# Optimization experiments

Measured on AMD Instinct MI355X. Metric: run time of the kernel, lower is better.

## Reference

```python
import jax, jax.numpy as jnp
import numpy as np

EMBED_DIM = 1024


def setup_inputs() -> dict:
    key = jax.random.key(0)
    ks = jax.random.split(key, 8)
    B, S, D = 4, 2048, EMBED_DIM
    scale = 1.0 / np.sqrt(D)
    x = jax.random.normal(ks[0], (B, S, D), dtype=jnp.float32)
    mask = jnp.zeros((S, S), dtype=jnp.float32)
    # nn.Linear default init ~ U(-1/sqrt(fan_in), 1/sqrt(fan_in)); exact dist irrelevant for correctness
    w_q = jax.random.uniform(ks[1], (D, D), jnp.float32, -scale, scale)
    b_q = jax.random.uniform(ks[2], (D,), jnp.float32, -scale, scale)
    w_k = jax.random.uniform(ks[3], (D, D), jnp.float32, -scale, scale)
    b_k = jax.random.uniform(ks[4], (D,), jnp.float32, -scale, scale)
    w_v = jax.random.uniform(ks[5], (D, D), jnp.float32, -scale, scale)
    b_v = jax.random.uniform(ks[6], (D,), jnp.float32, -scale, scale)
    return {"x": x, "mask": mask, "w_q": w_q, "b_q": b_q,
            "w_k": w_k, "b_k": b_k, "w_v": w_v, "b_v": b_v}


def reference(x, mask, w_q, b_q, w_k, b_k, w_v, b_v):
    D = x.shape[-1]
    # nn.Linear computes x @ W^T + b
    Q = jnp.einsum('bsd,ed->bse', x, w_q) + b_q
    K = jnp.einsum('bsd,ed->bse', x, w_k) + b_k
    V = jnp.einsum('bsd,ed->bse', x, w_v) + b_v
    scores = jnp.einsum('bqd,bkd->bqk', Q, K) / jnp.sqrt(jnp.asarray(D, x.dtype))
    scores = scores + mask  # additive mask, broadcast over batch
    attn = jax.nn.softmax(scores, axis=-1)
    return jnp.einsum('bqk,bkd->bqd', attn, V)
```

## Files before the change

kernel.cpp:

```cpp
#include <hip/hip_runtime.h>


typedef __attribute__((ext_vector_type(8))) short short8;
typedef __attribute__((ext_vector_type(4))) short short4v;
typedef __attribute__((ext_vector_type(4))) float float4v;

__device__ __forceinline__ short f2bf(float f) {
  unsigned u = __builtin_bit_cast(unsigned, f);
  u += 0x7fffu + ((u >> 16) & 1u);
  return (short)(u >> 16);
}

__device__ __forceinline__ void gl2lds16(const void* g, void* l) {
  __builtin_amdgcn_global_load_lds((const __attribute__((address_space(1))) void*)g,
                                   (__attribute__((address_space(3))) void*)l, 16, 0, 0);
}

__global__ __launch_bounds__(256) void cvt_kernel(const float* __restrict__ in,
                                                  short* __restrict__ out, int n4) {
  int i = blockIdx.x * 256 + threadIdx.x;
  if (i < n4) {
    float4v v = ((const float4v*)in)[i];
    short4v o;
    o.x = f2bf(v.x); o.y = f2bf(v.y); o.z = f2bf(v.z); o.w = f2bf(v.w);
    ((short4v*)out)[i] = o;
  }
}

__global__ __launch_bounds__(256) void prep_kernel(const float* __restrict__ wq,
                                                   const float* __restrict__ wk,
                                                   const float* __restrict__ wv,
                                                   const float* __restrict__ bq,
                                                   const float* __restrict__ bk,
                                                   const float* __restrict__ bv,
                                                   short* __restrict__ w_bf,
                                                   float* __restrict__ bcat) {
  int b = blockIdx.x;
  if (b < 3072) {
    int seg = b >> 10;
    const float* w = seg == 0 ? wq : (seg == 1 ? wk : wv);
    int i = (b - (seg << 10)) * 256 + threadIdx.x;
    float4v v = ((const float4v*)w)[i];
    short4v o;
    o.x = f2bf(v.x); o.y = f2bf(v.y); o.z = f2bf(v.z); o.w = f2bf(v.w);
    ((short4v*)(w_bf + (long)seg * 1048576))[i] = o;
  } else {
    int i = (b - 3072) * 256 + threadIdx.x;
    if (i < 3072) bcat[i] = i < 1024 ? bq[i] : (i < 2048 ? bk[i - 1024] : bv[i - 2048]);
  }
}

template <int EPI>
__global__ __launch_bounds__(256) void gemm_bt(const short* __restrict__ Aall,
                                               const short* __restrict__ Ball,
                                               void* __restrict__ Call,
                                               const float* __restrict__ aux, float scale,
                                               int M, int N, int Kd,
                                               long ab, long bb, long cb, long auxb) {
  const int bz = blockIdx.z;
  const short* A = Aall + (long)bz * ab;
  const short* Bm = Ball + (long)bz * bb;
  const float* auxp = aux + (long)bz * auxb;

  const int m0 = blockIdx.x * 128;
  const int n0 = blockIdx.y * 128;

  __shared__ alignas(16) short As[128][64];
  __shared__ alignas(16) short Bs[128][64];

  const int t = threadIdx.x;
  const int lane = t & 63, wave = t >> 6;
  const int wm = (wave & 1) * 64, wn = (wave >> 1) * 64;
  const int col = lane & 15, quad = lane >> 4;

  const int r_loc = lane >> 3;
  const int slot = lane & 7;
  const int cch = slot ^ r_loc;
  const int sw = col & 7;

  float4v acc[4][4] = {};
  float4v lacc[4] = {};
  short8 ones;
  if (EPI == 2) {
#pragma unroll
    for (int e = 0; e < 8; ++e) ones[e] = (short)0x3F80;
  }

  for (int kt = 0; kt < Kd; kt += 64) {
#pragma unroll
    for (int u = 0; u < 4; ++u) {
      const int rowbase = wave * 32 + u * 8;
      const int r = rowbase + r_loc;
      const long goff = (long)r * Kd + kt + cch * 8;
      short* lA = &As[rowbase][0] + lane * 8;
      short* lB = &Bs[rowbase][0] + lane * 8;
      gl2lds16(&A[(long)m0 * Kd + goff], lA);
      gl2lds16(&Bm[(long)n0 * Kd + goff], lB);
    }
    __syncthreads();

#pragma unroll
    for (int s = 0; s < 2; ++s) {
      short8 af[4], bfr[4];
#pragma unroll
      for (int i = 0; i < 4; ++i)
        af[i] = *(const short8*)&As[wm + i * 16 + col][((s * 4 + quad) ^ sw) * 8];
#pragma unroll
      for (int j = 0; j < 4; ++j)
        bfr[j] = *(const short8*)&Bs[wn + j * 16 + col][((s * 4 + quad) ^ sw) * 8];
#pragma unroll
      for (int i = 0; i < 4; ++i) {
#pragma unroll
        for (int j = 0; j < 4; ++j)
          acc[i][j] = __builtin_amdgcn_mfma_f32_16x16x32_bf16(af[i], bfr[j], acc[i][j], 0, 0, 0);
        if (EPI == 2)
          lacc[i] = __builtin_amdgcn_mfma_f32_16x16x32_bf16(af[i], ones, lacc[i], 0, 0, 0);
      }
    }
    __syncthreads();
  }

  const float LOG2E = 1.44269504f;
  const float c1 = scale * LOG2E;
#pragma unroll
  for (int i = 0; i < 4; ++i) {
    float4v inv;
    if (EPI == 2) {
#pragma unroll
      for (int r = 0; r < 4; ++r) inv[r] = 1.f / lacc[i][r];
    }
#pragma unroll
    for (int j = 0; j < 4; ++j) {
      const int n = n0 + wn + j * 16 + col;
      float addv = 0.f;
      if (EPI == 0) addv = auxp[n];
#pragma unroll
      for (int r = 0; r < 4; ++r) {
        const int m = m0 + wm + i * 16 + quad * 4 + r;
        float v = acc[i][j][r];
        if (EPI == 0) {
          ((short*)Call)[(long)bz * cb + (long)m * N + n] = f2bf(v + addv);
        } else if (EPI == 1) {
          float mv = auxp[(long)m * N + n];
          float e = exp2f(fmaf(v, c1, mv * LOG2E));
          ((short*)Call)[(long)bz * cb + (long)m * N + n] = f2bf(e);
        } else {
          ((float*)Call)[(long)bz * cb + (long)m * N + n] = v * inv[r];
        }
      }
    }
  }
}

__global__ __launch_bounds__(256) void transpose_v(const short* __restrict__ V,
                                                   short* __restrict__ Vt) {
  __shared__ short tile[32][33];
  const int b = blockIdx.z;
  const int s0 = blockIdx.x * 32, d0 = blockIdx.y * 32;
  const int tx = threadIdx.x & 31, ty = threadIdx.x >> 5;
  const short* src = V + (long)b * 2048 * 1024;
#pragma unroll
  for (int q = 0; q < 4; ++q) {
    int r = ty + q * 8;
    tile[r][tx] = src[(long)(s0 + r) * 1024 + d0 + tx];
  }
  __syncthreads();
  short* dst = Vt + (long)b * 1024 * 2048;
#pragma unroll
  for (int q = 0; q < 4; ++q) {
    int dr = ty + q * 8;
    dst[(long)(d0 + dr) * 2048 + s0 + tx] = tile[tx][dr];
  }
}

extern "C" void kernel_launch(void* const* d_in, const int* in_sizes, int n_in,
                              void* d_out, int out_size, void* d_ws, size_t ws_size,
                              hipStream_t stream) {
  const float* x    = (const float*)d_in[0];
  const float* mask = (const float*)d_in[1];
  const float* wq   = (const float*)d_in[2];
  const float* bq   = (const float*)d_in[3];
  const float* wk   = (const float*)d_in[4];
  const float* bk   = (const float*)d_in[5];
  const float* wv   = (const float*)d_in[6];
  const float* bv   = (const float*)d_in[7];
  float* out = (float*)d_out;

  char* ws = (char*)d_ws;
  const size_t MB = 1024 * 1024;
  short* x_bf = (short*)(ws);
  short* Vt   = (short*)(ws);
  short* w_bf = (short*)(ws + 16 * MB);
  short* QKV  = (short*)(ws + 22 * MB);
  short* P    = (short*)(ws + 70 * MB);
  float* bcat = (float*)(ws + 70 * MB);

  prep_kernel<<<3084, 256, 0, stream>>>(wq, wk, wv, bq, bk, bv, w_bf, bcat);
  cvt_kernel<<<8192, 256, 0, stream>>>(x, x_bf, 2097152);

  gemm_bt<0><<<dim3(64, 8, 3), 256, 0, stream>>>(x_bf, w_bf, QKV, bcat, 1.f,
                                                 8192, 1024, 1024,
                                                 0, 1048576, 8388608, 1024);

  short* Q  = QKV;
  short* Kb = QKV + 8388608;
  short* V  = QKV + 16777216;
  transpose_v<<<dim3(64, 32, 4), 256, 0, stream>>>(V, Vt);

  gemm_bt<1><<<dim3(16, 16, 4), 256, 0, stream>>>(Q, Kb, P, mask, 0.03125f,
                                                  2048, 2048, 1024,
                                                  2097152, 2097152, 4194304, 0);

  gemm_bt<2><<<dim3(16, 8, 4), 256, 0, stream>>>(P, Vt, out, nullptr, 1.f,
                                                 2048, 1024, 2048,
                                                 4194304, 2097152, 2097152, 0);
}
```

Baseline: 284.5 us.

## Use 32x32 MFMA, compute V transposed directly, and move row sums to a separate kernel

The GEMM inner loop switches from 16x16x32 to 32x32x16 bf16 MFMA with 2x2 accumulators per wave, which cuts LDS fragment reads per MFMA. V is now produced already transposed by a GEMM with W_v as the A operand and x as B, and a new epilogue adds the bias per row, so the separate transpose kernel goes away. The softmax denominator used to be computed with extra MFMAs against a ones vector. It now comes from a separate row-sum kernel over P, which adds one more pass over the P matrix in memory.

```diff
diff --git a/kernel.cpp b/kernel.cpp
--- a/kernel.cpp
+++ b/kernel.cpp
@@ -4,11 +4,16 @@
 typedef __attribute__((ext_vector_type(8))) short short8;
 typedef __attribute__((ext_vector_type(4))) short short4v;
 typedef __attribute__((ext_vector_type(4))) float float4v;
+typedef __attribute__((ext_vector_type(16))) float float16v;
 
 __device__ __forceinline__ short f2bf(float f) {
   unsigned u = __builtin_bit_cast(unsigned, f);
   u += 0x7fffu + ((u >> 16) & 1u);
   return (short)(u >> 16);
+}
+__device__ __forceinline__ float bf2f(short s) {
+  unsigned u = ((unsigned)(unsigned short)s) << 16;
+  return __builtin_bit_cast(float, u);
 }
 
 __device__ __forceinline__ void gl2lds16(const void* g, void* l) {
@@ -32,7 +37,6 @@
                                                    const float* __restrict__ wv,
                                                    const float* __restrict__ bq,
                                                    const float* __restrict__ bk,
-                                                   const float* __restrict__ bv,
                                                    short* __restrict__ w_bf,
                                                    float* __restrict__ bcat) {
   int b = blockIdx.x;
@@ -46,7 +50,7 @@
     ((short4v*)(w_bf + (long)seg * 1048576))[i] = o;
   } else {
     int i = (b - 3072) * 256 + threadIdx.x;
-    if (i < 3072) bcat[i] = i < 1024 ? bq[i] : (i < 2048 ? bk[i - 1024] : bv[i - 2048]);
+    if (i < 2048) bcat[i] = i < 1024 ? bq[i] : bk[i - 1024];
   }
 }
 
@@ -55,7 +59,7 @@
                                                const short* __restrict__ Ball,
                                                void* __restrict__ Call,
                                                const float* __restrict__ aux, float scale,
-                                               int M, int N, int Kd,
+                                               int M, int N, int Kd, int Bld,
                                                long ab, long bb, long cb, long auxb) {
   const int bz = blockIdx.z;
   const short* A = Aall + (long)bz * ab;
@@ -71,51 +75,40 @@
   const int t = threadIdx.x;
   const int lane = t & 63, wave = t >> 6;
   const int wm = (wave & 1) * 64, wn = (wave >> 1) * 64;
-  const int col = lane & 15, quad = lane >> 4;
+  const int col32 = lane & 31, half = lane >> 5;
 
   const int r_loc = lane >> 3;
   const int slot = lane & 7;
   const int cch = slot ^ r_loc;
-  const int sw = col & 7;
-
-  float4v acc[4][4] = {};
-  float4v lacc[4] = {};
-  short8 ones;
-  if (EPI == 2) {
-#pragma unroll
-    for (int e = 0; e < 8; ++e) ones[e] = (short)0x3F80;
-  }
+  const int sw = col32 & 7;
+
+  float16v acc[2][2] = {};
 
   for (int kt = 0; kt < Kd; kt += 64) {
 #pragma unroll
     for (int u = 0; u < 4; ++u) {
       const int rowbase = wave * 32 + u * 8;
       const int r = rowbase + r_loc;
-      const long goff = (long)r * Kd + kt + cch * 8;
-      short* lA = &As[rowbase][0] + lane * 8;
-      short* lB = &Bs[rowbase][0] + lane * 8;
-      gl2lds16(&A[(long)m0 * Kd + goff], lA);
-      gl2lds16(&Bm[(long)n0 * Kd + goff], lB);
+      gl2lds16(&A[(long)(m0 + r) * Kd + kt + cch * 8], &As[rowbase][0] + lane * 8);
+      gl2lds16(&Bm[(long)(n0 + r) * Bld + kt + cch * 8], &Bs[rowbase][0] + lane * 8);
     }
     __syncthreads();
 
 #pragma unroll
-    for (int s = 0; s < 2; ++s) {
-      short8 af[4], bfr[4];
-#pragma unroll
-      for (int i = 0; i < 4; ++i)
-        af[i] = *(const short8*)&As[wm + i * 16 + col][((s * 4 + quad) ^ sw) * 8];
-#pragma unroll
-      for (int j = 0; j < 4; ++j)
-        bfr[j] = *(const short8*)&Bs[wn + j * 16 + col][((s * 4 + quad) ^ sw) * 8];
-#pragma unroll
-      for (int i = 0; i < 4; ++i) {
-#pragma unroll
-        for (int j = 0; j < 4; ++j)
-          acc[i][j] = __builtin_amdgcn_mfma_f32_16x16x32_bf16(af[i], bfr[j], acc[i][j], 0, 0, 0);
-        if (EPI == 2)
-          lacc[i] = __builtin_amdgcn_mfma_f32_16x16x32_bf16(af[i], ones, lacc[i], 0, 0, 0);
-      }
+    for (int s = 0; s < 4; ++s) {
+      const int c = s * 2 + half;
+      short8 af[2], bfr[2];
+#pragma unroll
+      for (int i = 0; i < 2; ++i)
+        af[i] = *(const short8*)&As[wm + i * 32 + col32][(c ^ sw) * 8];
+#pragma unroll
+      for (int j = 0; j < 2; ++j)
+        bfr[j] = *(const short8*)&Bs[wn + j * 32 + col32][(c ^ sw) * 8];
+#pragma unroll
+      for (int i = 0; i < 2; ++i)
+#pragma unroll
+        for (int j = 0; j < 2; ++j)
+          acc[i][j] = __builtin_amdgcn_mfma_f32_32x32x16_bf16(af[i], bfr[j], acc[i][j], 0, 0, 0);
     }
     __syncthreads();
   }
@@ -123,54 +116,61 @@
   const float LOG2E = 1.44269504f;
   const float c1 = scale * LOG2E;
 #pragma unroll
-  for (int i = 0; i < 4; ++i) {
-    float4v inv;
+  for (int i = 0; i < 2; ++i) {
+    float invv[16], addm[16];
     if (EPI == 2) {
 #pragma unroll
-      for (int r = 0; r < 4; ++r) inv[r] = 1.f / lacc[i][r];
-    }
-#pragma unroll
-    for (int j = 0; j < 4; ++j) {
-      const int n = n0 + wn + j * 16 + col;
-      float addv = 0.f;
-      if (EPI == 0) addv = auxp[n];
-#pragma unroll
-      for (int r = 0; r < 4; ++r) {
-        const int m = m0 + wm + i * 16 + quad * 4 + r;
+      for (int r = 0; r < 16; ++r) {
+        const int m = m0 + wm + i * 32 + (r & 3) + 8 * (r >> 2) + 4 * half;
+        invv[r] = __builtin_amdgcn_rcpf(auxp[m]);
+      }
+    }
+    if (EPI == 3) {
+#pragma unroll
+      for (int r = 0; r < 16; ++r) {
+        const int m = m0 + wm + i * 32 + (r & 3) + 8 * (r >> 2) + 4 * half;
+        addm[r] = auxp[m];
+      }
+    }
+#pragma unroll
+    for (int j = 0; j < 2; ++j) {
+      const int n = n0 + wn + j * 32 + col32;
+      float addn = 0.f;
+      if (EPI == 0) addn = auxp[n];
+#pragma unroll
+      for (int r = 0; r < 16; ++r) {
+        const int m = m0 + wm + i * 32 + (r & 3) + 8 * (r >> 2) + 4 * half;
         float v = acc[i][j][r];
         if (EPI == 0) {
-          ((short*)Call)[(long)bz * cb + (long)m * N + n] = f2bf(v + addv);
+          ((short*)Call)[(long)bz * cb + (long)m * N + n] = f2bf(v + addn);
         } else if (EPI == 1) {
           float mv = auxp[(long)m * N + n];
           float e = exp2f(fmaf(v, c1, mv * LOG2E));
           ((short*)Call)[(long)bz * cb + (long)m * N + n] = f2bf(e);
+        } else if (EPI == 2) {
+          ((float*)Call)[(long)bz * cb + (long)m * N + n] = v * invv[r];
         } else {
-          ((float*)Call)[(long)bz * cb + (long)m * N + n] = v * inv[r];
+          ((short*)Call)[(long)bz * cb + (long)m * N + n] = f2bf(v + addm[r]);
         }
       }
     }
   }
 }
 
-__global__ __launch_bounds__(256) void transpose_v(const short* __restrict__ V,
-                                                   short* __restrict__ Vt) {
-  __shared__ short tile[32][33];
-  const int b = blockIdx.z;
-  const int s0 = blockIdx.x * 32, d0 = blockIdx.y * 32;
-  const int tx = threadIdx.x & 31, ty = threadIdx.x >> 5;
-  const short* src = V + (long)b * 2048 * 1024;
-#pragma unroll
-  for (int q = 0; q < 4; ++q) {
-    int r = ty + q * 8;
-    tile[r][tx] = src[(long)(s0 + r) * 1024 + d0 + tx];
-  }
+__global__ __launch_bounds__(256) void rowsum_kernel(const short* __restrict__ P,
+                                                     float* __restrict__ rs) {
+  const long row = blockIdx.x;
+  const int t = threadIdx.x;
+  short8 raw = *(const short8*)(P + row * 2048 + t * 8);
+  float s = 0.f;
+#pragma unroll
+  for (int e = 0; e < 8; ++e) s += bf2f(raw[e]);
+#pragma unroll
+  for (int off = 32; off > 0; off >>= 1) s += __shfl_xor(s, off);
+  __shared__ float red[4];
+  if ((t & 63) == 0) red[t >> 6] = s;
   __syncthreads();
-  short* dst = Vt + (long)b * 1024 * 2048;
-#pragma unroll
-  for (int q = 0; q < 4; ++q) {
-    int dr = ty + q * 8;
-    dst[(long)(d0 + dr) * 2048 + s0 + tx] = tile[tx][dr];
-  }
+  if (t == 0) rs[row] = red[0] + red[1] + red[2] + red[3];
 }
 
 extern "C" void kernel_launch(void* const* d_in, const int* in_sizes, int n_in,
@@ -189,29 +189,34 @@
   char* ws = (char*)d_ws;
   const size_t MB = 1024 * 1024;
   short* x_bf = (short*)(ws);
-  short* Vt   = (short*)(ws);
   short* w_bf = (short*)(ws + 16 * MB);
-  short* QKV  = (short*)(ws + 22 * MB);
+  float* rs   = (float*)(ws + 16 * MB);
+  short* QK   = (short*)(ws + 22 * MB);
+  short* Vt   = (short*)(ws + 54 * MB);
   short* P    = (short*)(ws + 70 * MB);
   float* bcat = (float*)(ws + 70 * MB);
 
-  prep_kernel<<<3084, 256, 0, stream>>>(wq, wk, wv, bq, bk, bv, w_bf, bcat);
+  prep_kernel<<<3080, 256, 0, stream>>>(wq, wk, wv, bq, bk, w_bf, bcat);
   cvt_kernel<<<8192, 256, 0, stream>>>(x, x_bf, 2097152);
 
-  gemm_bt<0><<<dim3(64, 8, 3), 256, 0, stream>>>(x_bf, w_bf, QKV, bcat, 1.f,
-                                                 8192, 1024, 1024,
+  gemm_bt<0><<<dim3(64, 8, 2), 256, 0, stream>>>(x_bf, w_bf, QK, bcat, 1.f,
+                                                 8192, 1024, 1024, 1024,
                                                  0, 1048576, 8388608, 1024);
 
-  short* Q  = QKV;
-  short* Kb = QKV + 8388608;
-  short* V  = QKV + 16777216;
-  transpose_v<<<dim3(64, 32, 4), 256, 0, stream>>>(V, Vt);
+  gemm_bt<3><<<dim3(8, 64, 1), 256, 0, stream>>>(w_bf + 2097152, x_bf, Vt, bv, 1.f,
+                                                 1024, 8192, 1024, 1024,
+                                                 0, 0, 0, 0);
+
+  short* Q  = QK;
+  short* Kb = QK + 8388608;
 
   gemm_bt<1><<<dim3(16, 16, 4), 256, 0, stream>>>(Q, Kb, P, mask, 0.03125f,
-                                                  2048, 2048, 1024,
+                                                  2048, 2048, 1024, 1024,
                                                   2097152, 2097152, 4194304, 0);
 
-  gemm_bt<2><<<dim3(16, 8, 4), 256, 0, stream>>>(P, Vt, out, nullptr, 1.f,
-                                                 2048, 1024, 2048,
-                                                 4194304, 2097152, 2097152, 0);
-}
+  rowsum_kernel<<<8192, 256, 0, stream>>>(P, rs);
+
+  gemm_bt<2><<<dim3(16, 8, 4), 256, 0, stream>>>(P, Vt, out, rs, 1.f,
+                                                 2048, 1024, 2048, 8192,
+                                                 4194304, 2048, 2097152, 2048);
+}
```

Measured after the change: 277.9 us. -2.3%, faster.
